# Kernel optimization log

Measured on AMD Instinct MI355X. Metric: run time of the kernel, lower is better.

The kernel has to match this reference:

```python
import jax, jax.numpy as jnp
import numpy as np

N_NODES = 50000
N_EDGES = 800000
IN_CH = 256
OUT_CH = 128
HID = 2 * OUT_CH  # 256
LN_EPS = 1e-5


def _add_self_loops(edge_index, n):
    loop = jnp.arange(n, dtype=edge_index.dtype)
    src = jnp.concatenate([edge_index[0], loop])
    dst = jnp.concatenate([edge_index[1], loop])
    return src, dst


def _gcn_norm(src, dst, n):
    # PyG GCNConv norm: deg over source index, symmetric normalization
    ones = jnp.ones(src.shape[0], dtype=jnp.float32)
    deg = jax.ops.segment_sum(ones, src, num_segments=n)
    dinv = jnp.where(deg > 0, deg ** -0.5, 0.0)
    return dinv[src] * dinv[dst]  # [E+N]


def _gcn_conv(x, src, dst, norm, w, b, gamma=None, beta=None):
    h = x @ w                              # [N, out]
    msgs = norm[:, None] * h[src]          # gather + scale, [E+N, out]
    out = jax.ops.segment_sum(msgs, dst, num_segments=x.shape[0])
    if gamma is not None:
        out = gamma * out + beta           # FiLM modulation (per-feature)
    return out + b


def _layernorm(x):
    mu = jnp.mean(x, axis=-1, keepdims=True)
    var = jnp.var(x, axis=-1, keepdims=True)
    return (x - mu) * jax.lax.rsqrt(var + LN_EPS)


def setup_inputs() -> dict:
    key = jax.random.key(0)
    ks = jax.random.split(key, 20)

    def g(k, shape, scale=0.05):
        return jax.random.normal(k, shape, dtype=jnp.float32) * scale

    x = jax.random.normal(ks[0], (N_NODES, IN_CH), dtype=jnp.float32)
    edge_index = jax.random.randint(ks[1], (2, N_EDGES), 0, N_NODES, dtype=jnp.int64)
    return {
        "x": x,
        "edge_index": edge_index,
        "conv1_w": g(ks[2], (IN_CH, HID)),
        "conv1_b": g(ks[3], (HID,)),
        "conv2_w": g(ks[4], (HID, OUT_CH)),
        "conv2_b": g(ks[5], (OUT_CH,)),
        "sig_conv_w": g(ks[6], (IN_CH, HID)),
        "sig_conv_b": g(ks[7], (HID,)),
        "fc1_w": g(ks[8], (HID, HID)),
        "fc1_b": g(ks[9], (HID,)),
        "fc2_w": g(ks[10], (HID, HID)),
        "fc2_b": g(ks[11], (HID,)),
        "fc3_w": g(ks[12], (OUT_CH, HID)),
        "fc3_b": g(ks[13], (OUT_CH,)),
        "fc4_w": g(ks[14], (OUT_CH, HID)),
        "fc4_b": g(ks[15], (OUT_CH,)),
    }


def reference(x, edge_index, conv1_w, conv1_b, conv2_w, conv2_b,
              sig_conv_w, sig_conv_b, fc1_w, fc1_b, fc2_w, fc2_b,
              fc3_w, fc3_b, fc4_w, fc4_b):
    n = x.shape[0]
    src, dst = _add_self_loops(edge_index, n)
    norm = _gcn_norm(src, dst, n)

    # --- GraphSignature (use_gcn_sig=True) ---
    s = jax.nn.relu(_gcn_conv(x, src, dst, norm, sig_conv_w, sig_conv_b))
    s = s.sum(0)  # [HID]
    gamma1 = jnp.tanh(s @ fc1_w.T + fc1_b)  # [HID]
    beta1 = jnp.tanh(s @ fc2_w.T + fc2_b)   # [HID]
    gamma2 = jnp.tanh(s @ fc3_w.T + fc3_b)  # [OUT]
    beta2 = jnp.tanh(s @ fc4_w.T + fc4_b)   # [OUT]

    # inner_loop=True: signature outputs are detached
    gamma1, beta1, gamma2, beta2 = map(jax.lax.stop_gradient,
                                       (gamma1, beta1, gamma2, beta2))

    # --- Encoder (GAE) ---
    h = jax.nn.relu(_gcn_conv(x, src, dst, norm, conv1_w, conv1_b,
                              gamma=gamma1, beta=beta1))
    h = _layernorm(h)
    out = _gcn_conv(h, src, dst, norm, conv2_w, conv2_b,
                    gamma=gamma2, beta=beta2)
    out = _layernorm(out)
    return out
```

## Files before the change

kernel.cpp:

```cpp
#include <hip/hip_runtime.h>

typedef _Float16 f16;
typedef f16 f16x8 __attribute__((ext_vector_type(8)));
typedef float f32x4 __attribute__((ext_vector_type(4)));
typedef unsigned short u16;

#define IN_CH  256
#define HID    256
#define OUT_CH 128
#define LN_EPS 1e-5f
#define NSLOT  32
#define NR     4
#define NC     64
#define RS     12544
#define HT     512


__global__ __launch_bounds__(HT) void k_hist(const int* __restrict__ ei, int nE, int nN,
                                             int* __restrict__ hP) {
    __shared__ int h[RS];
    int r = blockIdx.x & (NR - 1), c = blockIdx.x >> 2;
    int rsz = (nN + NR - 1) / NR;
    int r0 = r * rsz;
    int sz = nN - r0; if (sz > rsz) sz = rsz;
    for (int i = threadIdx.x; i < sz; i += HT) h[i] = 0;
    __syncthreads();
    int nT = nE + nN;
    int chunk = (nT + NC - 1) / NC;
    int e0 = c * chunk, e1 = e0 + chunk; if (e1 > nT) e1 = nT;
    for (int eb = e0 + (int)threadIdx.x; eb < e1; eb += HT * 4) {
        int ss[4], dd[4];
        #pragma unroll
        for (int u = 0; u < 4; u++) {
            int e = eb + u * HT;
            ss[u] = -1; dd[u] = -1;
            if (e < e1) {
                if (e < nE) { ss[u] = ei[e]; dd[u] = ei[nE + e]; }
                else { ss[u] = e - nE; dd[u] = e - nE; }
            }
        }
        #pragma unroll
        for (int u = 0; u < 4; u++) {
            if ((unsigned)(ss[u] - r0) < (unsigned)sz) atomicAdd(&h[ss[u] - r0], 1);
            if ((unsigned)(dd[u] - r0) < (unsigned)sz) atomicAdd(&h[dd[u] - r0], 0x10000);
        }
    }
    __syncthreads();
    for (int i = threadIdx.x; i < sz; i += HT) hP[(size_t)c * nN + r0 + i] = h[i];
}


__global__ __launch_bounds__(256) void k_alloc(const int* __restrict__ hP,
                                               int* __restrict__ rowstart,
                                               int* __restrict__ chunkbase,
                                               int* __restrict__ cnt_tot,
                                               float* __restrict__ dinv,
                                               int* __restrict__ ctr, int nN,
                                               const float* __restrict__ x, f16* __restrict__ xh,
                                               int nelem, int nAllocB, int nCast,
                                               const float* __restrict__ sigw,
                                               const float* __restrict__ c1w,
                                               const float* __restrict__ c2w,
                                               f16* __restrict__ Wt1, f16* __restrict__ Wt2) {
    int bid = blockIdx.x;
    if (bid < nAllocB) {
        int i = bid * 256 + threadIdx.x;
        int lane = threadIdx.x & 63;
        int cnt = 0, dg = 0;
        if (i < nN) {
            for (int c = 0; c < NC; c++) {
                unsigned pk = (unsigned)hP[(size_t)c * nN + i];
                cnt += (int)(pk >> 16);
                dg  += (int)(pk & 0xffffu);
            }
        }
        int p = cnt;
        #pragma unroll
        for (int off = 1; off < 64; off <<= 1) {
            int v = __shfl_up(p, off, 64);
            if (lane >= off) p += v;
        }
        int tot = __shfl(p, 63, 64);
        int base = 0;
        if (lane == 0) base = atomicAdd(ctr, tot);
        base = __shfl(base, 0, 64);
        if (i < nN) {
            int nb = base + p - cnt;
            rowstart[i] = nb;
            cnt_tot[i] = cnt;
            dinv[i] = rsqrtf((float)dg);
            int run = nb;
            for (int c = 0; c < NC; c++) {
                chunkbase[(size_t)c * nN + i] = run;
                run += (int)((unsigned)hP[(size_t)c * nN + i] >> 16);
            }
        }
    } else if (bid < nAllocB + nCast) {
        int i = (bid - nAllocB) * 2048 + threadIdx.x * 8;
        if (i >= nelem) return;
        float4 a = *(const float4*)(x + i);
        float4 b = *(const float4*)(x + i + 4);
        f16x8 o = { (f16)a.x, (f16)a.y, (f16)a.z, (f16)a.w,
                    (f16)b.x, (f16)b.y, (f16)b.z, (f16)b.w };
        *(f16x8*)(xh + i) = o;
    } else {
        int i = (bid - nAllocB - nCast) * 256 + threadIdx.x;
        if (i < 512 * 256) {
            int n = i >> 8, k = i & 255;
            float v = (n < 256) ? sigw[k * 256 + n] : c1w[k * 256 + (n - 256)];
            Wt1[(size_t)n * 256 + k] = (f16)v;
        } else {
            int j = i - 512 * 256;
            if (j < 128 * 256) {
                int n = j >> 8, k = j & 255;
                Wt2[(size_t)n * 256 + k] = (f16)c2w[k * 128 + n];
            }
        }
    }
}


__global__ __launch_bounds__(HT) void k_fill(const int* __restrict__ ei, int nE, int nN,
                                             const int* __restrict__ chunkbase,
                                             u16* __restrict__ src_sorted) {
    __shared__ int pos_[RS];
    int r = blockIdx.x & (NR - 1), c = blockIdx.x >> 2;
    int rsz = (nN + NR - 1) / NR;
    int r0 = r * rsz;
    int sz = nN - r0; if (sz > rsz) sz = rsz;
    for (int i = threadIdx.x; i < sz; i += HT)
        pos_[i] = chunkbase[(size_t)c * nN + r0 + i];
    __syncthreads();
    int nT = nE + nN;
    int chunk = (nT + NC - 1) / NC;
    int e0 = c * chunk, e1 = e0 + chunk; if (e1 > nT) e1 = nT;
    for (int eb = e0 + (int)threadIdx.x; eb < e1; eb += HT * 4) {
        int ss[4], dd[4];
        #pragma unroll
        for (int u = 0; u < 4; u++) {
            int e = eb + u * HT;
            ss[u] = -1; dd[u] = -1;
            if (e < e1) {
                if (e < nE) { ss[u] = ei[e]; dd[u] = ei[nE + e]; }
                else { ss[u] = e - nE; dd[u] = e - nE; }
            }
        }
        #pragma unroll
        for (int u = 0; u < 4; u++) {
            int l = dd[u] - r0;
            if ((unsigned)l < (unsigned)sz) {
                int pos = atomicAdd(&pos_[l], 1);
                src_sorted[pos] = (u16)ss[u];
            }
        }
    }
}


__global__ __launch_bounds__(256) void k_aggX(const f16* __restrict__ xh,
                                              const int* __restrict__ rowstart,
                                              const int* __restrict__ counts,
                                              const u16* __restrict__ srcs,
                                              const float* __restrict__ dinv,
                                              f16* __restrict__ AX, int nN) {
    int wv = threadIdx.x >> 6;
    int lane = threadIdx.x & 63;
    int node = blockIdx.x * 4 + wv;
    if (node >= nN) return;
    int h = lane >> 5, sub = lane & 31;
    int beg = rowstart[node];
    int cnt = counts[node];
    float acc0[8] = {}, acc1[8] = {};
    for (int base = 0; base < cnt; base += 64) {
        int el = base + lane;
        int sv = 0; float dv = 0.f;
        if (el < cnt) { sv = srcs[beg + el]; dv = dinv[sv]; }
        int rem = cnt - base; if (rem > 64) rem = 64;
        for (int e = 0; e < rem; e += 8) {
            int i0 = e + h, i1 = e + 2 + h, i2 = e + 4 + h, i3 = e + 6 + h;
            int sa = __shfl(sv, i0, 64), sb = __shfl(sv, i1, 64);
            int sc = __shfl(sv, i2, 64), sd = __shfl(sv, i3, 64);
            float na = __shfl(dv, i0, 64), nb = __shfl(dv, i1, 64);
            float nc = __shfl(dv, i2, 64), nd = __shfl(dv, i3, 64);
            if (i0 >= rem) na = 0.f;
            if (i1 >= rem) nb = 0.f;
            if (i2 >= rem) nc = 0.f;
            if (i3 >= rem) nd = 0.f;
            f16x8 va = *(const f16x8*)(xh + (size_t)sa * 256 + sub * 8);
            f16x8 vb = *(const f16x8*)(xh + (size_t)sb * 256 + sub * 8);
            f16x8 vc = *(const f16x8*)(xh + (size_t)sc * 256 + sub * 8);
            f16x8 vd = *(const f16x8*)(xh + (size_t)sd * 256 + sub * 8);
            #pragma unroll
            for (int j = 0; j < 8; j++) {
                acc0[j] = fmaf(na, (float)va[j], acc0[j]);
                acc1[j] = fmaf(nb, (float)vb[j], acc1[j]);
                acc0[j] = fmaf(nc, (float)vc[j], acc0[j]);
                acc1[j] = fmaf(nd, (float)vd[j], acc1[j]);
            }
        }
    }
    float dn = dinv[node];
    #pragma unroll
    for (int j = 0; j < 8; j++) {
        acc0[j] += acc1[j];
        acc0[j] += __shfl_xor(acc0[j], 32, 64);
    }
    if (lane < 32) {
        f16x8 o;
        #pragma unroll
        for (int j = 0; j < 8; j++) o[j] = (f16)(acc0[j] * dn);
        *(f16x8*)(AX + (size_t)node * 256 + sub * 8) = o;
    }
}


__global__ __launch_bounds__(256) void k_gemm_sig(const f16* __restrict__ AX,
                                                  const f16* __restrict__ Wt,
                                                  const float* __restrict__ sigb,
                                                  float* __restrict__ sig_part, int M) {
    __shared__ float tile[32][257];
    int t = threadIdx.x;
    int w = t >> 6, lane = t & 63, quad = lane >> 4, l16 = lane & 15;
    int m0 = blockIdx.x * 32;
    int cb = w * 64;
    f32x4 acc[2][4] = {};
    for (int kk = 0; kk < 256; kk += 32) {
        int ka = kk + quad * 8;
        f16x8 a[2];
        #pragma unroll
        for (int ms = 0; ms < 2; ms++) {
            int row = m0 + ms * 16 + l16; if (row >= M) row = M - 1;
            a[ms] = *(const f16x8*)(AX + (size_t)row * 256 + ka);
        }
        #pragma unroll
        for (int ns = 0; ns < 4; ns++) {
            f16x8 b = *(const f16x8*)(Wt + (size_t)(cb + ns * 16 + l16) * 256 + ka);
            acc[0][ns] = __builtin_amdgcn_mfma_f32_16x16x32_f16(a[0], b, acc[0][ns], 0, 0, 0);
            acc[1][ns] = __builtin_amdgcn_mfma_f32_16x16x32_f16(a[1], b, acc[1][ns], 0, 0, 0);
        }
    }
    #pragma unroll
    for (int ms = 0; ms < 2; ms++)
        #pragma unroll
        for (int ns = 0; ns < 4; ns++)
            #pragma unroll
            for (int r = 0; r < 4; r++) {
                int mr = ms * 16 + quad * 4 + r;
                int c = cb + ns * 16 + l16;
                float v = fmaxf(acc[ms][ns][r] + sigb[c], 0.f);
                if (m0 + mr >= M) v = 0.f;
                tile[mr][c] = v;
            }
    __syncthreads();
    float s = 0.f;
    #pragma unroll 8
    for (int r = 0; r < 32; r++) s += tile[r][t];
    atomicAdd(&sig_part[(blockIdx.x & (NSLOT - 1)) * 256 + t], s);
}


__global__ __launch_bounds__(256) void k_fc(const float* __restrict__ sig_part,
                                            const float* __restrict__ f1w, const float* __restrict__ f1b,
                                            const float* __restrict__ f2w, const float* __restrict__ f2b,
                                            const float* __restrict__ f3w, const float* __restrict__ f3b,
                                            const float* __restrict__ f4w, const float* __restrict__ f4b,
                                            float* __restrict__ g1, float* __restrict__ b1,
                                            float* __restrict__ g2, float* __restrict__ b2) {
    __shared__ float ss[256];
    int t = threadIdx.x;
    float s = 0.f;
    for (int k = 0; k < NSLOT; k++) s += sig_part[k * 256 + t];
    ss[t] = s;
    __syncthreads();
    int wv = t >> 6, lane = t & 63;
    float s0 = ss[lane], s1 = ss[lane + 64], s2v = ss[lane + 128], s3 = ss[lane + 192];
    #pragma unroll
    for (int rr = 0; rr < 16; rr++) {
        int row = blockIdx.x * 64 + wv * 16 + rr;
        const float* w; const float* bb; float* dst; int r;
        if (row < 256)      { w = f1w; bb = f1b; dst = g1; r = row; }
        else if (row < 512) { w = f2w; bb = f2b; dst = b1; r = row - 256; }
        else if (row < 640) { w = f3w; bb = f3b; dst = g2; r = row - 512; }
        else                { w = f4w; bb = f4b; dst = b2; r = row - 640; }
        const float* wr = w + (size_t)r * 256;
        float a = wr[lane] * s0;
        a = fmaf(wr[lane + 64], s1, a);
        a = fmaf(wr[lane + 128], s2v, a);
        a = fmaf(wr[lane + 192], s3, a);
        #pragma unroll
        for (int off = 1; off < 64; off <<= 1) a += __shfl_xor(a, off, 64);
        if (lane == 0) dst[r] = tanhf(a + bb[r]);
    }
}


__global__ __launch_bounds__(256) void k_c1f(const f16* __restrict__ AX,
                                             const f16* __restrict__ Wt,
                                             const f16* __restrict__ Wt2,
                                             const float* __restrict__ g1,
                                             const float* __restrict__ b1,
                                             const float* __restrict__ c1b,
                                             const float* __restrict__ dinv,
                                             f16* __restrict__ HW, int M) {
    __shared__ float tile[32][257];
    __shared__ f16 ht[32][264];
    __shared__ float ps[8][33], ps2[8][33];
    __shared__ float mu_[32], rr_[32], sdinv[32];
    int t = threadIdx.x;
    int w = t >> 6, lane = t & 63, quad = lane >> 4, l16 = lane & 15;
    int m0 = blockIdx.x * 32;
    int cb = w * 64;
    f32x4 acc[2][4] = {};
    for (int kk = 0; kk < 256; kk += 32) {
        int ka = kk + quad * 8;
        f16x8 a[2];
        #pragma unroll
        for (int ms = 0; ms < 2; ms++) {
            int row = m0 + ms * 16 + l16; if (row >= M) row = M - 1;
            a[ms] = *(const f16x8*)(AX + (size_t)row * 256 + ka);
        }
        #pragma unroll
        for (int ns = 0; ns < 4; ns++) {
            f16x8 b = *(const f16x8*)(Wt + (size_t)(cb + ns * 16 + l16) * 256 + ka);
            acc[0][ns] = __builtin_amdgcn_mfma_f32_16x16x32_f16(a[0], b, acc[0][ns], 0, 0, 0);
            acc[1][ns] = __builtin_amdgcn_mfma_f32_16x16x32_f16(a[1], b, acc[1][ns], 0, 0, 0);
        }
    }
    #pragma unroll
    for (int ms = 0; ms < 2; ms++)
        #pragma unroll
        for (int ns = 0; ns < 4; ns++)
            #pragma unroll
            for (int r = 0; r < 4; r++) {
                int mr = ms * 16 + quad * 4 + r;
                int c = cb + ns * 16 + l16;
                tile[mr][c] = fmaxf(fmaf(g1[c], acc[ms][ns][r], b1[c] + c1b[c]), 0.f);
            }
    __syncthreads();
    {
        int r = t & 31, seg = t >> 5;
        float s = 0.f, s2 = 0.f;
        #pragma unroll 8
        for (int c = seg * 32; c < seg * 32 + 32; c++) {
            float xv = tile[r][c];
            s += xv; s2 = fmaf(xv, xv, s2);
        }
        ps[seg][r] = s; ps2[seg][r] = s2;
    }
    __syncthreads();
    if (t < 32) {
        float S = 0.f, S2 = 0.f;
        #pragma unroll
        for (int g = 0; g < 8; g++) { S += ps[g][t]; S2 += ps2[g][t]; }
        float mu = S * (1.f / 256.f);
        mu_[t] = mu;
        rr_[t] = rsqrtf(S2 * (1.f / 256.f) - mu * mu + LN_EPS);
        int m = m0 + t;
        sdinv[t] = (m < M) ? dinv[m] : 0.f;
    }
    __syncthreads();
    #pragma unroll 8
    for (int r = 0; r < 32; r++)
        ht[r][t] = (f16)((tile[r][t] - mu_[r]) * rr_[r]);
    __syncthreads();
    int cb2 = w * 32;
    f32x4 acc2[2][2] = {};
    for (int kk = 0; kk < 256; kk += 32) {
        int ka = kk + quad * 8;
        f16x8 a[2];
        #pragma unroll
        for (int ms = 0; ms < 2; ms++)
            a[ms] = *(const f16x8*)(&ht[ms * 16 + l16][ka]);
        #pragma unroll
        for (int ns = 0; ns < 2; ns++) {
            f16x8 b = *(const f16x8*)(Wt2 + (size_t)(cb2 + ns * 16 + l16) * 256 + ka);
            acc2[0][ns] = __builtin_amdgcn_mfma_f32_16x16x32_f16(a[0], b, acc2[0][ns], 0, 0, 0);
            acc2[1][ns] = __builtin_amdgcn_mfma_f32_16x16x32_f16(a[1], b, acc2[1][ns], 0, 0, 0);
        }
    }
    #pragma unroll
    for (int ms = 0; ms < 2; ms++)
        #pragma unroll
        for (int ns = 0; ns < 2; ns++)
            #pragma unroll
            for (int r = 0; r < 4; r++) {
                int mr = ms * 16 + quad * 4 + r;
                int m = m0 + mr;
                if (m < M) HW[(size_t)m * 128 + cb2 + ns * 16 + l16] = (f16)(acc2[ms][ns][r] * sdinv[mr]);
            }
}


__global__ __launch_bounds__(256) void k_agg2(const f16* __restrict__ HW,
                                              const int* __restrict__ rowstart,
                                              const int* __restrict__ counts,
                                              const u16* __restrict__ srcs,
                                              const float* __restrict__ dinv,
                                              const float* __restrict__ g2,
                                              const float* __restrict__ b2,
                                              const float* __restrict__ c2b,
                                              float* __restrict__ out, int nN) {
    int wv = threadIdx.x >> 6;
    int lane = threadIdx.x & 63;
    int node = blockIdx.x * 4 + wv;
    if (node >= nN) return;
    int q = lane >> 4, sub = lane & 15;
    int beg = rowstart[node];
    int cnt = counts[node];
    float acc0[8] = {}, acc1[8] = {};
    for (int base = 0; base < cnt; base += 64) {
        int el = base + lane;
        int sv = 0; float dv = 0.f;
        if (el < cnt) { sv = srcs[beg + el]; dv = 1.f; }
        int rem = cnt - base; if (rem > 64) rem = 64;
        for (int e = 0; e < rem; e += 8) {
            int i0 = e + q, i1 = e + 4 + q;
            int sa = __shfl(sv, i0, 64), sb = __shfl(sv, i1, 64);
            float na = __shfl(dv, i0, 64), nb = __shfl(dv, i1, 64);
            if (i0 >= rem) na = 0.f;
            if (i1 >= rem) nb = 0.f;
            f16x8 va = *(const f16x8*)(HW + (size_t)sa * 128 + sub * 8);
            f16x8 vb = *(const f16x8*)(HW + (size_t)sb * 128 + sub * 8);
            #pragma unroll
            for (int j = 0; j < 8; j++) {
                acc0[j] = fmaf(na, (float)va[j], acc0[j]);
                acc1[j] = fmaf(nb, (float)vb[j], acc1[j]);
            }
        }
    }
    float dn = dinv[node];
    #pragma unroll
    for (int j = 0; j < 8; j++) {
        acc0[j] += acc1[j];
        acc0[j] += __shfl_xor(acc0[j], 16, 64);
        acc0[j] += __shfl_xor(acc0[j], 32, 64);
    }
    int ch = sub * 8;
    float vfin[8];
    float s = 0.f, s2 = 0.f;
    #pragma unroll
    for (int j = 0; j < 8; j++) {
        float v = fmaf(g2[ch + j], acc0[j] * dn, b2[ch + j] + c2b[ch + j]);
        vfin[j] = v;
        s += v; s2 = fmaf(v, v, s2);
    }
    #pragma unroll
    for (int off = 1; off < 16; off <<= 1) {
        s += __shfl_xor(s, off, 64);
        s2 += __shfl_xor(s2, off, 64);
    }
    float mu = s * (1.f / 128.f);
    float rr = rsqrtf(s2 * (1.f / 128.f) - mu * mu + LN_EPS);
    if (q == 0) {
        float4 o0 = { (vfin[0] - mu) * rr, (vfin[1] - mu) * rr,
                      (vfin[2] - mu) * rr, (vfin[3] - mu) * rr };
        float4 o1 = { (vfin[4] - mu) * rr, (vfin[5] - mu) * rr,
                      (vfin[6] - mu) * rr, (vfin[7] - mu) * rr };
        float* dst = out + (size_t)node * 128 + ch;
        *(float4*)dst = o0;
        *(float4*)(dst + 4) = o1;
    }
}


extern "C" void kernel_launch(void* const* d_in, const int* in_sizes, int n_in,
                              void* d_out, int out_size, void* d_ws, size_t ws_size,
                              hipStream_t stream) {
    const float* x    = (const float*)d_in[0];
    const int*   ei   = (const int*)d_in[1];
    const float* c1w  = (const float*)d_in[2];
    const float* c1b  = (const float*)d_in[3];
    const float* c2w  = (const float*)d_in[4];
    const float* c2b  = (const float*)d_in[5];
    const float* sigw = (const float*)d_in[6];
    const float* sigb = (const float*)d_in[7];
    const float* f1w  = (const float*)d_in[8];
    const float* f1b  = (const float*)d_in[9];
    const float* f2w  = (const float*)d_in[10];
    const float* f2b  = (const float*)d_in[11];
    const float* f3w  = (const float*)d_in[12];
    const float* f3b  = (const float*)d_in[13];
    const float* f4w  = (const float*)d_in[14];
    const float* f4b  = (const float*)d_in[15];
    float* out = (float*)d_out;

    int nN = in_sizes[0] / IN_CH;
    int nE = in_sizes[1] / 2;
    int nT = nE + nN;

    char* base = (char*)d_ws;
    size_t off = 0;
    auto alloc = [&](size_t bytes) { size_t o = off; off += (bytes + 255) & ~(size_t)255; return o; };

    size_t o_spart  = alloc((size_t)NSLOT * 256 * 4);
    size_t o_ctr    = alloc(256);
    size_t zero_bytes = off;
    size_t o_hP     = alloc((size_t)NC * nN * 4);
    size_t o_cbase  = alloc((size_t)NC * nN * 4);
    size_t o_g1     = alloc(256 * 4);
    size_t o_b1     = alloc(256 * 4);
    size_t o_g2     = alloc(128 * 4);
    size_t o_b2     = alloc(128 * 4);
    size_t o_rowst  = alloc((size_t)nN * 4);
    size_t o_cntt   = alloc((size_t)nN * 4);
    size_t o_dinv   = alloc((size_t)nN * 4);
    size_t o_src    = alloc((size_t)nT * 2);
    size_t o_wt1    = alloc(512 * 256 * 2);
    size_t o_wt2    = alloc(128 * 256 * 2);
    size_t o_xh     = alloc((size_t)nN * 256 * 2);
    size_t o_AX     = alloc((size_t)nN * 256 * 2);
    size_t o_HW     = alloc((size_t)nN * 128 * 2);

    float* spart  = (float*)(base + o_spart);
    int*   ctr    = (int*)(base + o_ctr);
    int*   hP     = (int*)(base + o_hP);
    int*   cbase  = (int*)(base + o_cbase);
    float* g1     = (float*)(base + o_g1);
    float* b1     = (float*)(base + o_b1);
    float* g2     = (float*)(base + o_g2);
    float* b2     = (float*)(base + o_b2);
    int*   rowst  = (int*)(base + o_rowst);
    int*   cntt   = (int*)(base + o_cntt);
    float* dinv   = (float*)(base + o_dinv);
    u16*   srcs   = (u16*)(base + o_src);
    f16*   Wt1    = (f16*)(base + o_wt1);
    f16*   Wt2    = (f16*)(base + o_wt2);
    f16*   xh     = (f16*)(base + o_xh);
    f16*   AX     = (f16*)(base + o_AX);
    f16*   HW     = (f16*)(base + o_HW);

    hipMemsetAsync(base, 0, zero_bytes, stream);

    k_hist<<<NR * NC, HT, 0, stream>>>(ei, nE, nN, hP);

    int nAllocB = (nN + 255) / 256;
    int nCast = (nN * IN_CH + 2047) / 2048;
    int nPrep = (512 * 256 + 128 * 256) / 256;
    k_alloc<<<nAllocB + nCast + nPrep, 256, 0, stream>>>(hP, rowst, cbase, cntt, dinv, ctr, nN,
                                                         x, xh, nN * IN_CH, nAllocB, nCast,
                                                         sigw, c1w, c2w, Wt1, Wt2);

    k_fill<<<NR * NC, HT, 0, stream>>>(ei, nE, nN, cbase, srcs);

    int nb4 = (nN + 3) / 4;
    int mg = (nN + 31) / 32;
    k_aggX<<<nb4, 256, 0, stream>>>(xh, rowst, cntt, srcs, dinv, AX, nN);
    k_gemm_sig<<<mg, 256, 0, stream>>>(AX, Wt1, sigb, spart, nN);
    k_fc<<<12, 256, 0, stream>>>(spart, f1w, f1b, f2w, f2b, f3w, f3b, f4w, f4b, g1, b1, g2, b2);
    k_c1f<<<mg, 256, 0, stream>>>(AX, Wt1 + 256 * 256, Wt2, g1, b1, c1b, dinv, HW, nN);
    k_agg2<<<nb4, 256, 0, stream>>>(HW, rowst, cntt, srcs, dinv, g2, b2, c2b, out, nN);
}
```

Measured before the change: 363.6 us.

## Restructure dense GEMMs so each wave owns 16 nodes across all channels

Both dense GEMM kernels now compute a 64-node tile in which each wave holds 16 nodes times all 256 output channels in registers, with weights as the A operand and node rows as B. In the fused conv1 kernel, LayerNorm statistics are reduced with in-wave shuffles, and the normalized activations are re-packed into MFMA operands through shuffles rather than going through shared memory, which removes several __syncthreads and LDS tiles. The conv biases are folded into the FiLM beta vectors inside k_fc. The cost is much higher register pressure from 16 accumulator vectors, which may reduce occupancy, and the signature tile is stored in f16, lowering precision of the column sum.

```diff
diff --git a/kernel.cpp b/kernel.cpp
--- a/kernel.cpp
+++ b/kernel.cpp
@@ -4,6 +4,7 @@
 typedef f16 f16x8 __attribute__((ext_vector_type(8)));
 typedef float f32x4 __attribute__((ext_vector_type(4)));
 typedef unsigned short u16;
+typedef unsigned int u32;
 
 #define IN_CH  256
 #define HID    256
@@ -218,43 +219,37 @@
                                                   const f16* __restrict__ Wt,
                                                   const float* __restrict__ sigb,
                                                   float* __restrict__ sig_part, int M) {
-    __shared__ float tile[32][257];
+    __shared__ f16 tile[64][264];
     int t = threadIdx.x;
     int w = t >> 6, lane = t & 63, quad = lane >> 4, l16 = lane & 15;
-    int m0 = blockIdx.x * 32;
-    int cb = w * 64;
-    f32x4 acc[2][4] = {};
+    int node = blockIdx.x * 64 + w * 16 + l16;
+    int nrow = node < M ? node : M - 1;
+    const f16* axp = AX + (size_t)nrow * 256;
+    f32x4 acc[16] = {};
     for (int kk = 0; kk < 256; kk += 32) {
-        int ka = kk + quad * 8;
-        f16x8 a[2];
-        #pragma unroll
-        for (int ms = 0; ms < 2; ms++) {
-            int row = m0 + ms * 16 + l16; if (row >= M) row = M - 1;
-            a[ms] = *(const f16x8*)(AX + (size_t)row * 256 + ka);
-        }
-        #pragma unroll
-        for (int ns = 0; ns < 4; ns++) {
-            f16x8 b = *(const f16x8*)(Wt + (size_t)(cb + ns * 16 + l16) * 256 + ka);
-            acc[0][ns] = __builtin_amdgcn_mfma_f32_16x16x32_f16(a[0], b, acc[0][ns], 0, 0, 0);
-            acc[1][ns] = __builtin_amdgcn_mfma_f32_16x16x32_f16(a[1], b, acc[1][ns], 0, 0, 0);
-        }
-    }
-    #pragma unroll
-    for (int ms = 0; ms < 2; ms++)
-        #pragma unroll
-        for (int ns = 0; ns < 4; ns++)
-            #pragma unroll
-            for (int r = 0; r < 4; r++) {
-                int mr = ms * 16 + quad * 4 + r;
-                int c = cb + ns * 16 + l16;
-                float v = fmaxf(acc[ms][ns][r] + sigb[c], 0.f);
-                if (m0 + mr >= M) v = 0.f;
-                tile[mr][c] = v;
-            }
+        f16x8 bfrag = *(const f16x8*)(axp + kk + quad * 8);
+        #pragma unroll
+        for (int ct = 0; ct < 16; ct++) {
+            f16x8 afrag = *(const f16x8*)(Wt + (size_t)(ct * 16 + l16) * 256 + kk + quad * 8);
+            acc[ct] = __builtin_amdgcn_mfma_f32_16x16x32_f16(afrag, bfrag, acc[ct], 0, 0, 0);
+        }
+    }
+    bool valid = node < M;
+    #pragma unroll
+    for (int ct = 0; ct < 16; ct++) {
+        f32x4 sb4 = *(const f32x4*)(sigb + ct * 16 + quad * 4);
+        union { f16 h[4]; uint2 u2; } p;
+        #pragma unroll
+        for (int r = 0; r < 4; r++) {
+            float v = fmaxf(acc[ct][r] + sb4[r], 0.f);
+            p.h[r] = valid ? (f16)v : (f16)0.f;
+        }
+        *(uint2*)(&tile[w * 16 + l16][ct * 16 + quad * 4]) = p.u2;
+    }
     __syncthreads();
     float s = 0.f;
     #pragma unroll 8
-    for (int r = 0; r < 32; r++) s += tile[r][t];
+    for (int r = 0; r < 64; r++) s += (float)tile[r][t];
     atomicAdd(&sig_part[(blockIdx.x & (NSLOT - 1)) * 256 + t], s);
 }
 
@@ -264,8 +259,9 @@
                                             const float* __restrict__ f2w, const float* __restrict__ f2b,
                                             const float* __restrict__ f3w, const float* __restrict__ f3b,
                                             const float* __restrict__ f4w, const float* __restrict__ f4b,
-                                            float* __restrict__ g1, float* __restrict__ b1,
-                                            float* __restrict__ g2, float* __restrict__ b2) {
+                                            const float* __restrict__ c1b, const float* __restrict__ c2b,
+                                            float* __restrict__ g1, float* __restrict__ bc1,
+                                            float* __restrict__ g2, float* __restrict__ bc2) {
     __shared__ float ss[256];
     int t = threadIdx.x;
     float s = 0.f;
@@ -277,11 +273,11 @@
     #pragma unroll
     for (int rr = 0; rr < 16; rr++) {
         int row = blockIdx.x * 64 + wv * 16 + rr;
-        const float* w; const float* bb; float* dst; int r;
-        if (row < 256)      { w = f1w; bb = f1b; dst = g1; r = row; }
-        else if (row < 512) { w = f2w; bb = f2b; dst = b1; r = row - 256; }
-        else if (row < 640) { w = f3w; bb = f3b; dst = g2; r = row - 512; }
-        else                { w = f4w; bb = f4b; dst = b2; r = row - 640; }
+        const float* w; const float* bb; const float* ex; float* dst; int r;
+        if (row < 256)      { w = f1w; bb = f1b; dst = g1;  ex = 0;   r = row; }
+        else if (row < 512) { w = f2w; bb = f2b; dst = bc1; ex = c1b; r = row - 256; }
+        else if (row < 640) { w = f3w; bb = f3b; dst = g2;  ex = 0;   r = row - 512; }
+        else                { w = f4w; bb = f4b; dst = bc2; ex = c2b; r = row - 640; }
         const float* wr = w + (size_t)r * 256;
         float a = wr[lane] * s0;
         a = fmaf(wr[lane + 64], s1, a);
@@ -289,7 +285,7 @@
         a = fmaf(wr[lane + 192], s3, a);
         #pragma unroll
         for (int off = 1; off < 64; off <<= 1) a += __shfl_xor(a, off, 64);
-        if (lane == 0) dst[r] = tanhf(a + bb[r]);
+        if (lane == 0) dst[r] = tanhf(a + bb[r]) + (ex ? ex[r] : 0.f);
     }
 }
 
@@ -298,96 +294,86 @@
                                              const f16* __restrict__ Wt,
                                              const f16* __restrict__ Wt2,
                                              const float* __restrict__ g1,
-                                             const float* __restrict__ b1,
-                                             const float* __restrict__ c1b,
+                                             const float* __restrict__ bc1,
                                              const float* __restrict__ dinv,
                                              f16* __restrict__ HW, int M) {
-    __shared__ float tile[32][257];
-    __shared__ f16 ht[32][264];
-    __shared__ float ps[8][33], ps2[8][33];
-    __shared__ float mu_[32], rr_[32], sdinv[32];
     int t = threadIdx.x;
     int w = t >> 6, lane = t & 63, quad = lane >> 4, l16 = lane & 15;
-    int m0 = blockIdx.x * 32;
-    int cb = w * 64;
-    f32x4 acc[2][4] = {};
+    int node = blockIdx.x * 64 + w * 16 + l16;
+    int nrow = node < M ? node : M - 1;
+    const f16* axp = AX + (size_t)nrow * 256;
+
+    f32x4 acc[16] = {};
     for (int kk = 0; kk < 256; kk += 32) {
-        int ka = kk + quad * 8;
-        f16x8 a[2];
-        #pragma unroll
-        for (int ms = 0; ms < 2; ms++) {
-            int row = m0 + ms * 16 + l16; if (row >= M) row = M - 1;
-            a[ms] = *(const f16x8*)(AX + (size_t)row * 256 + ka);
-        }
-        #pragma unroll
-        for (int ns = 0; ns < 4; ns++) {
-            f16x8 b = *(const f16x8*)(Wt + (size_t)(cb + ns * 16 + l16) * 256 + ka);
-            acc[0][ns] = __builtin_amdgcn_mfma_f32_16x16x32_f16(a[0], b, acc[0][ns], 0, 0, 0);
-            acc[1][ns] = __builtin_amdgcn_mfma_f32_16x16x32_f16(a[1], b, acc[1][ns], 0, 0, 0);
-        }
-    }
-    #pragma unroll
-    for (int ms = 0; ms < 2; ms++)
-        #pragma unroll
-        for (int ns = 0; ns < 4; ns++)
+        f16x8 bfrag = *(const f16x8*)(axp + kk + quad * 8);
+        #pragma unroll
+        for (int ct = 0; ct < 16; ct++) {
+            f16x8 afrag = *(const f16x8*)(Wt + (size_t)(ct * 16 + l16) * 256 + kk + quad * 8);
+            acc[ct] = __builtin_amdgcn_mfma_f32_16x16x32_f16(afrag, bfrag, acc[ct], 0, 0, 0);
+        }
+    }
+
+    float s = 0.f, s2 = 0.f;
+    #pragma unroll
+    for (int ct = 0; ct < 16; ct++) {
+        f32x4 gv = *(const f32x4*)(g1 + ct * 16 + quad * 4);
+        f32x4 bv = *(const f32x4*)(bc1 + ct * 16 + quad * 4);
+        #pragma unroll
+        for (int r = 0; r < 4; r++) {
+            float v = fmaxf(fmaf(gv[r], acc[ct][r], bv[r]), 0.f);
+            acc[ct][r] = v;
+            s += v; s2 = fmaf(v, v, s2);
+        }
+    }
+    s  += __shfl_xor(s, 16, 64);  s  += __shfl_xor(s, 32, 64);
+    s2 += __shfl_xor(s2, 16, 64); s2 += __shfl_xor(s2, 32, 64);
+    float mu = s * (1.f / 256.f);
+    float rr = rsqrtf(s2 * (1.f / 256.f) - mu * mu + LN_EPS);
+
+    u32 Plo[16], Phi[16];
+    #pragma unroll
+    for (int ct = 0; ct < 16; ct++) {
+        union { f16 h[4]; u32 u[2]; } p;
+        #pragma unroll
+        for (int r = 0; r < 4; r++) p.h[r] = (f16)((acc[ct][r] - mu) * rr);
+        Plo[ct] = p.u[0]; Phi[ct] = p.u[1];
+    }
+
+    bool hi = (lane & 32) != 0;
+    int idx0 = ((quad & 1) << 5) + l16;
+    f32x4 acc2[8] = {};
+    #pragma unroll
+    for (int ts = 0; ts < 8; ts++) {
+        u32 a0lo = (u32)__shfl((int)Plo[2 * ts], idx0, 64);
+        u32 a0hi = (u32)__shfl((int)Phi[2 * ts], idx0, 64);
+        u32 b0lo = (u32)__shfl((int)Plo[2 * ts + 1], idx0, 64);
+        u32 b0hi = (u32)__shfl((int)Phi[2 * ts + 1], idx0, 64);
+        u32 a1lo = (u32)__shfl((int)Plo[2 * ts], idx0 + 16, 64);
+        u32 a1hi = (u32)__shfl((int)Phi[2 * ts], idx0 + 16, 64);
+        u32 b1lo = (u32)__shfl((int)Plo[2 * ts + 1], idx0 + 16, 64);
+        u32 b1hi = (u32)__shfl((int)Phi[2 * ts + 1], idx0 + 16, 64);
+        union { u32 u[4]; f16x8 v; } bf;
+        bf.u[0] = hi ? b0lo : a0lo;
+        bf.u[1] = hi ? b0hi : a0hi;
+        bf.u[2] = hi ? b1lo : a1lo;
+        bf.u[3] = hi ? b1hi : a1hi;
+        #pragma unroll
+        for (int nt2 = 0; nt2 < 8; nt2++) {
+            f16x8 afrag = *(const f16x8*)(Wt2 + (size_t)(nt2 * 16 + l16) * 256 + ts * 32 + quad * 8);
+            acc2[nt2] = __builtin_amdgcn_mfma_f32_16x16x32_f16(afrag, bf.v, acc2[nt2], 0, 0, 0);
+        }
+    }
+
+    if (node < M) {
+        float dn = dinv[node];
+        #pragma unroll
+        for (int nt2 = 0; nt2 < 8; nt2++) {
+            union { f16 h[4]; uint2 u2; } o;
             #pragma unroll
-            for (int r = 0; r < 4; r++) {
-                int mr = ms * 16 + quad * 4 + r;
-                int c = cb + ns * 16 + l16;
-                tile[mr][c] = fmaxf(fmaf(g1[c], acc[ms][ns][r], b1[c] + c1b[c]), 0.f);
-            }
-    __syncthreads();
-    {
-        int r = t & 31, seg = t >> 5;
-        float s = 0.f, s2 = 0.f;
-        #pragma unroll 8
-        for (int c = seg * 32; c < seg * 32 + 32; c++) {
-            float xv = tile[r][c];
-            s += xv; s2 = fmaf(xv, xv, s2);
-        }
-        ps[seg][r] = s; ps2[seg][r] = s2;
-    }
-    __syncthreads();
-    if (t < 32) {
-        float S = 0.f, S2 = 0.f;
-        #pragma unroll
-        for (int g = 0; g < 8; g++) { S += ps[g][t]; S2 += ps2[g][t]; }
-        float mu = S * (1.f / 256.f);
-        mu_[t] = mu;
-        rr_[t] = rsqrtf(S2 * (1.f / 256.f) - mu * mu + LN_EPS);
-        int m = m0 + t;
-        sdinv[t] = (m < M) ? dinv[m] : 0.f;
-    }
-    __syncthreads();
-    #pragma unroll 8
-    for (int r = 0; r < 32; r++)
-        ht[r][t] = (f16)((tile[r][t] - mu_[r]) * rr_[r]);
-    __syncthreads();
-    int cb2 = w * 32;
-    f32x4 acc2[2][2] = {};
-    for (int kk = 0; kk < 256; kk += 32) {
-        int ka = kk + quad * 8;
-        f16x8 a[2];
-        #pragma unroll
-        for (int ms = 0; ms < 2; ms++)
-            a[ms] = *(const f16x8*)(&ht[ms * 16 + l16][ka]);
-        #pragma unroll
-        for (int ns = 0; ns < 2; ns++) {
-            f16x8 b = *(const f16x8*)(Wt2 + (size_t)(cb2 + ns * 16 + l16) * 256 + ka);
-            acc2[0][ns] = __builtin_amdgcn_mfma_f32_16x16x32_f16(a[0], b, acc2[0][ns], 0, 0, 0);
-            acc2[1][ns] = __builtin_amdgcn_mfma_f32_16x16x32_f16(a[1], b, acc2[1][ns], 0, 0, 0);
-        }
-    }
-    #pragma unroll
-    for (int ms = 0; ms < 2; ms++)
-        #pragma unroll
-        for (int ns = 0; ns < 2; ns++)
-            #pragma unroll
-            for (int r = 0; r < 4; r++) {
-                int mr = ms * 16 + quad * 4 + r;
-                int m = m0 + mr;
-                if (m < M) HW[(size_t)m * 128 + cb2 + ns * 16 + l16] = (f16)(acc2[ms][ns][r] * sdinv[mr]);
-            }
+            for (int r = 0; r < 4; r++) o.h[r] = (f16)(acc2[nt2][r] * dn);
+            *(uint2*)(HW + (size_t)node * 128 + nt2 * 16 + quad * 4) = o.u2;
+        }
+    }
 }
 
 
@@ -397,8 +383,7 @@
                                               const u16* __restrict__ srcs,
                                               const float* __restrict__ dinv,
                                               const float* __restrict__ g2,
-                                              const float* __restrict__ b2,
-                                              const float* __restrict__ c2b,
+                                              const float* __restrict__ bc2,
                                               float* __restrict__ out, int nN) {
     int wv = threadIdx.x >> 6;
     int lane = threadIdx.x & 63;
@@ -440,7 +425,7 @@
     float s = 0.f, s2 = 0.f;
     #pragma unroll
     for (int j = 0; j < 8; j++) {
-        float v = fmaf(g2[ch + j], acc0[j] * dn, b2[ch + j] + c2b[ch + j]);
+        float v = fmaf(g2[ch + j], acc0[j] * dn, bc2[ch + j]);
         vfin[j] = v;
         s += v; s2 = fmaf(v, v, s2);
     }
@@ -516,9 +501,9 @@
     int*   hP     = (int*)(base + o_hP);
     int*   cbase  = (int*)(base + o_cbase);
     float* g1     = (float*)(base + o_g1);
-    float* b1     = (float*)(base + o_b1);
+    float* bc1    = (float*)(base + o_b1);
     float* g2     = (float*)(base + o_g2);
-    float* b2     = (float*)(base + o_b2);
+    float* bc2    = (float*)(base + o_b2);
     int*   rowst  = (int*)(base + o_rowst);
     int*   cntt   = (int*)(base + o_cntt);
     float* dinv   = (float*)(base + o_dinv);
@@ -543,10 +528,11 @@
     k_fill<<<NR * NC, HT, 0, stream>>>(ei, nE, nN, cbase, srcs);
 
     int nb4 = (nN + 3) / 4;
-    int mg = (nN + 31) / 32;
+    int mg64 = (nN + 63) / 64;
     k_aggX<<<nb4, 256, 0, stream>>>(xh, rowst, cntt, srcs, dinv, AX, nN);
-    k_gemm_sig<<<mg, 256, 0, stream>>>(AX, Wt1, sigb, spart, nN);
-    k_fc<<<12, 256, 0, stream>>>(spart, f1w, f1b, f2w, f2b, f3w, f3b, f4w, f4b, g1, b1, g2, b2);
-    k_c1f<<<mg, 256, 0, stream>>>(AX, Wt1 + 256 * 256, Wt2, g1, b1, c1b, dinv, HW, nN);
-    k_agg2<<<nb4, 256, 0, stream>>>(HW, rowst, cntt, srcs, dinv, g2, b2, c2b, out, nN);
-}
+    k_gemm_sig<<<mg64, 256, 0, stream>>>(AX, Wt1, sigb, spart, nN);
+    k_fc<<<12, 256, 0, stream>>>(spart, f1w, f1b, f2w, f2b, f3w, f3b, f4w, f4b,
+                                 c1b, c2b, g1, bc1, g2, bc2);
+    k_c1f<<<mg64, 256, 0, stream>>>(AX, Wt1 + 256 * 256, Wt2, g1, bc1, dinv, HW, nN);
+    k_agg2<<<nb4, 256, 0, stream>>>(HW, rowst, cntt, srcs, dinv, g2, bc2, out, nN);
+}
```

New measurement: 429.3 us. 1.18x slower.

## Compute LayerNorm stats in registers and shrink shared-memory tiles in GEMM kernels

Applied to the files above, without the earlier changes.

In the first-layer fused kernel, row sums and sums of squares are now reduced from the MFMA accumulators with lane shuffles instead of going through a 32x257 float shared tile. Normalization then writes f16 directly from registers, which removes about 33 KB of LDS per block and one barrier. The signature GEMM's reduction tile moves from float to f16 to halve its LDS footprint. Conv biases are folded into the beta vectors inside the fc kernel so later kernels load one bias array. The f16 tile in the signature sum loses precision before the column reduction.

```diff
diff --git a/kernel.cpp b/kernel.cpp
--- a/kernel.cpp
+++ b/kernel.cpp
@@ -4,6 +4,7 @@
 typedef f16 f16x8 __attribute__((ext_vector_type(8)));
 typedef float f32x4 __attribute__((ext_vector_type(4)));
 typedef unsigned short u16;
+typedef unsigned int u32;
 
 #define IN_CH  256
 #define HID    256
@@ -218,7 +219,7 @@
                                                   const f16* __restrict__ Wt,
                                                   const float* __restrict__ sigb,
                                                   float* __restrict__ sig_part, int M) {
-    __shared__ float tile[32][257];
+    __shared__ f16 tile[32][264];
     int t = threadIdx.x;
     int w = t >> 6, lane = t & 63, quad = lane >> 4, l16 = lane & 15;
     int m0 = blockIdx.x * 32;
@@ -249,12 +250,12 @@
                 int c = cb + ns * 16 + l16;
                 float v = fmaxf(acc[ms][ns][r] + sigb[c], 0.f);
                 if (m0 + mr >= M) v = 0.f;
-                tile[mr][c] = v;
+                tile[mr][c] = (f16)v;
             }
     __syncthreads();
     float s = 0.f;
     #pragma unroll 8
-    for (int r = 0; r < 32; r++) s += tile[r][t];
+    for (int r = 0; r < 32; r++) s += (float)tile[r][t];
     atomicAdd(&sig_part[(blockIdx.x & (NSLOT - 1)) * 256 + t], s);
 }
 
@@ -264,8 +265,9 @@
                                             const float* __restrict__ f2w, const float* __restrict__ f2b,
                                             const float* __restrict__ f3w, const float* __restrict__ f3b,
                                             const float* __restrict__ f4w, const float* __restrict__ f4b,
-                                            float* __restrict__ g1, float* __restrict__ b1,
-                                            float* __restrict__ g2, float* __restrict__ b2) {
+                                            const float* __restrict__ c1b, const float* __restrict__ c2b,
+                                            float* __restrict__ g1, float* __restrict__ bc1,
+                                            float* __restrict__ g2, float* __restrict__ bc2) {
     __shared__ float ss[256];
     int t = threadIdx.x;
     float s = 0.f;
@@ -277,11 +279,11 @@
     #pragma unroll
     for (int rr = 0; rr < 16; rr++) {
         int row = blockIdx.x * 64 + wv * 16 + rr;
-        const float* w; const float* bb; float* dst; int r;
-        if (row < 256)      { w = f1w; bb = f1b; dst = g1; r = row; }
-        else if (row < 512) { w = f2w; bb = f2b; dst = b1; r = row - 256; }
-        else if (row < 640) { w = f3w; bb = f3b; dst = g2; r = row - 512; }
-        else                { w = f4w; bb = f4b; dst = b2; r = row - 640; }
+        const float* w; const float* bb; const float* ex; float* dst; int r;
+        if (row < 256)      { w = f1w; bb = f1b; dst = g1;  ex = 0;   r = row; }
+        else if (row < 512) { w = f2w; bb = f2b; dst = bc1; ex = c1b; r = row - 256; }
+        else if (row < 640) { w = f3w; bb = f3b; dst = g2;  ex = 0;   r = row - 512; }
+        else                { w = f4w; bb = f4b; dst = bc2; ex = c2b; r = row - 640; }
         const float* wr = w + (size_t)r * 256;
         float a = wr[lane] * s0;
         a = fmaf(wr[lane + 64], s1, a);
@@ -289,7 +291,7 @@
         a = fmaf(wr[lane + 192], s3, a);
         #pragma unroll
         for (int off = 1; off < 64; off <<= 1) a += __shfl_xor(a, off, 64);
-        if (lane == 0) dst[r] = tanhf(a + bb[r]);
+        if (lane == 0) dst[r] = tanhf(a + bb[r]) + (ex ? ex[r] : 0.f);
     }
 }
 
@@ -298,13 +300,11 @@
                                              const f16* __restrict__ Wt,
                                              const f16* __restrict__ Wt2,
                                              const float* __restrict__ g1,
-                                             const float* __restrict__ b1,
-                                             const float* __restrict__ c1b,
+                                             const float* __restrict__ bc1,
                                              const float* __restrict__ dinv,
                                              f16* __restrict__ HW, int M) {
-    __shared__ float tile[32][257];
     __shared__ f16 ht[32][264];
-    __shared__ float ps[8][33], ps2[8][33];
+    __shared__ float ps[32][5], ps2[32][5];
     __shared__ float mu_[32], rr_[32], sdinv[32];
     int t = threadIdx.x;
     int w = t >> 6, lane = t & 63, quad = lane >> 4, l16 = lane & 15;
@@ -326,32 +326,46 @@
             acc[1][ns] = __builtin_amdgcn_mfma_f32_16x16x32_f16(a[1], b, acc[1][ns], 0, 0, 0);
         }
     }
-    #pragma unroll
-    for (int ms = 0; ms < 2; ms++)
-        #pragma unroll
-        for (int ns = 0; ns < 4; ns++)
+
+    float rs[2][4] = {{0.f,0.f,0.f,0.f},{0.f,0.f,0.f,0.f}};
+    float rs2[2][4] = {{0.f,0.f,0.f,0.f},{0.f,0.f,0.f,0.f}};
+    #pragma unroll
+    for (int ns = 0; ns < 4; ns++) {
+        int c = cb + ns * 16 + l16;
+        float gv = g1[c], bv = bc1[c];
+        #pragma unroll
+        for (int ms = 0; ms < 2; ms++)
+            #pragma unroll
+            for (int r = 0; r < 4; r++) {
+                float v = fmaxf(fmaf(gv, acc[ms][ns][r], bv), 0.f);
+                acc[ms][ns][r] = v;
+                rs[ms][r] += v;
+                rs2[ms][r] = fmaf(v, v, rs2[ms][r]);
+            }
+    }
+    #pragma unroll
+    for (int off = 1; off < 16; off <<= 1)
+        #pragma unroll
+        for (int ms = 0; ms < 2; ms++)
+            #pragma unroll
+            for (int r = 0; r < 4; r++) {
+                rs[ms][r]  += __shfl_xor(rs[ms][r], off, 64);
+                rs2[ms][r] += __shfl_xor(rs2[ms][r], off, 64);
+            }
+    if (l16 == 0) {
+        #pragma unroll
+        for (int ms = 0; ms < 2; ms++)
             #pragma unroll
             for (int r = 0; r < 4; r++) {
                 int mr = ms * 16 + quad * 4 + r;
-                int c = cb + ns * 16 + l16;
-                tile[mr][c] = fmaxf(fmaf(g1[c], acc[ms][ns][r], b1[c] + c1b[c]), 0.f);
-            }
-    __syncthreads();
-    {
-        int r = t & 31, seg = t >> 5;
-        float s = 0.f, s2 = 0.f;
-        #pragma unroll 8
-        for (int c = seg * 32; c < seg * 32 + 32; c++) {
-            float xv = tile[r][c];
-            s += xv; s2 = fmaf(xv, xv, s2);
-        }
-        ps[seg][r] = s; ps2[seg][r] = s2;
+                ps[mr][w] = rs[ms][r];
+                ps2[mr][w] = rs2[ms][r];
+            }
     }
     __syncthreads();
     if (t < 32) {
-        float S = 0.f, S2 = 0.f;
-        #pragma unroll
-        for (int g = 0; g < 8; g++) { S += ps[g][t]; S2 += ps2[g][t]; }
+        float S = ps[t][0] + ps[t][1] + ps[t][2] + ps[t][3];
+        float S2 = ps2[t][0] + ps2[t][1] + ps2[t][2] + ps2[t][3];
         float mu = S * (1.f / 256.f);
         mu_[t] = mu;
         rr_[t] = rsqrtf(S2 * (1.f / 256.f) - mu * mu + LN_EPS);
@@ -359,9 +373,16 @@
         sdinv[t] = (m < M) ? dinv[m] : 0.f;
     }
     __syncthreads();
-    #pragma unroll 8
-    for (int r = 0; r < 32; r++)
-        ht[r][t] = (f16)((tile[r][t] - mu_[r]) * rr_[r]);
+    #pragma unroll
+    for (int ms = 0; ms < 2; ms++)
+        #pragma unroll
+        for (int r = 0; r < 4; r++) {
+            int mr = ms * 16 + quad * 4 + r;
+            float mu = mu_[mr], rr = rr_[mr];
+            #pragma unroll
+            for (int ns = 0; ns < 4; ns++)
+                ht[mr][cb + ns * 16 + l16] = (f16)((acc[ms][ns][r] - mu) * rr);
+        }
     __syncthreads();
     int cb2 = w * 32;
     f32x4 acc2[2][2] = {};
@@ -397,8 +418,7 @@
                                               const u16* __restrict__ srcs,
                                               const float* __restrict__ dinv,
                                               const float* __restrict__ g2,
-                                              const float* __restrict__ b2,
-                                              const float* __restrict__ c2b,
+                                              const float* __restrict__ bc2,
                                               float* __restrict__ out, int nN) {
     int wv = threadIdx.x >> 6;
     int lane = threadIdx.x & 63;
@@ -440,7 +460,7 @@
     float s = 0.f, s2 = 0.f;
     #pragma unroll
     for (int j = 0; j < 8; j++) {
-        float v = fmaf(g2[ch + j], acc0[j] * dn, b2[ch + j] + c2b[ch + j]);
+        float v = fmaf(g2[ch + j], acc0[j] * dn, bc2[ch + j]);
         vfin[j] = v;
         s += v; s2 = fmaf(v, v, s2);
     }
@@ -516,9 +536,9 @@
     int*   hP     = (int*)(base + o_hP);
     int*   cbase  = (int*)(base + o_cbase);
     float* g1     = (float*)(base + o_g1);
-    float* b1     = (float*)(base + o_b1);
+    float* bc1    = (float*)(base + o_b1);
     float* g2     = (float*)(base + o_g2);
-    float* b2     = (float*)(base + o_b2);
+    float* bc2    = (float*)(base + o_b2);
     int*   rowst  = (int*)(base + o_rowst);
     int*   cntt   = (int*)(base + o_cntt);
     float* dinv   = (float*)(base + o_dinv);
@@ -546,7 +566,8 @@
     int mg = (nN + 31) / 32;
     k_aggX<<<nb4, 256, 0, stream>>>(xh, rowst, cntt, srcs, dinv, AX, nN);
     k_gemm_sig<<<mg, 256, 0, stream>>>(AX, Wt1, sigb, spart, nN);
-    k_fc<<<12, 256, 0, stream>>>(spart, f1w, f1b, f2w, f2b, f3w, f3b, f4w, f4b, g1, b1, g2, b2);
-    k_c1f<<<mg, 256, 0, stream>>>(AX, Wt1 + 256 * 256, Wt2, g1, b1, c1b, dinv, HW, nN);
-    k_agg2<<<nb4, 256, 0, stream>>>(HW, rowst, cntt, srcs, dinv, g2, b2, c2b, out, nN);
-}
+    k_fc<<<12, 256, 0, stream>>>(spart, f1w, f1b, f2w, f2b, f3w, f3b, f4w, f4b,
+                                 c1b, c2b, g1, bc1, g2, bc2);
+    k_c1f<<<mg, 256, 0, stream>>>(AX, Wt1 + 256 * 256, Wt2, g1, bc1, dinv, HW, nN);
+    k_agg2<<<nb4, 256, 0, stream>>>(HW, rowst, cntt, srcs, dinv, g2, bc2, out, nN);
+}
```

Result: no change. 365.1 us (+0.4%).
